# Performance work log

Measured on AMD Instinct MI355X. Metric: run time of the kernel, lower is better.

## Reference

```python
import jax, jax.numpy as jnp
import numpy as np

N_HEAD = 16
TEMPERATURE = 1.0

def setup_inputs() -> dict:
    key = jax.random.key(0)
    ks = jax.random.split(key, 5)
    B, L, D = 2, 2048, 1024
    s = 0.02
    return {
        'x':     jax.random.normal(ks[0], (B, L, D), jnp.float32),
        'q_g':   jax.random.normal(ks[1], (B, L, D), jnp.float32),
        'k_g':   jax.random.normal(ks[2], (B, L, D), jnp.float32),
        'W_qkv': jax.random.normal(ks[3], (D, 3 * D), jnp.float32) * s,
        'W_out': jax.random.normal(ks[4], (D, D), jnp.float32) * s,
    }

def reference(x, q_g, k_g, W_qkv, W_out):
    B, L, D = x.shape
    H = N_HEAD
    hd = D // H
    qkv = x @ W_qkv                                    # [B, L, 3D]
    q, k, v = jnp.split(qkv, 3, axis=-1)
    def to_heads(t):                                    # [B,L,D] -> [B,H,L,hd]
        return t.reshape(B, L, H, hd).transpose(0, 2, 1, 3)
    q, k, v = to_heads(q), to_heads(k), to_heads(v)
    qg, kg = to_heads(q_g), to_heads(k_g)

    scale = 1.0 / jnp.sqrt(jnp.float32(hd))
    # dual score matrices (same math as concat-on-head-dim then split)
    aw_x = jnp.einsum('bhqd,bhkd->bhqk', q, k) * scale    # [B,H,L,L]
    aw_g = jnp.einsum('bhqd,bhkd->bhqk', qg, kg) * scale  # [B,H,L,L]
    # sensory_attention=True, merge='add'
    attn = aw_x + aw_g

    causal = jnp.tril(jnp.ones((L, L), dtype=bool))
    attn = jnp.where(causal, attn, -jnp.inf)
    log_norm = jnp.log(jnp.float32(L))                    # softmax_log_norm=True
    attn = jax.nn.softmax(attn / (log_norm * TEMPERATURE), axis=-1)

    y = jnp.einsum('bhqk,bhkd->bhqd', attn, v)            # [B,H,L,hd]
    y = y.transpose(0, 2, 1, 3).reshape(B, L, D)
    return y @ W_out
```

## Files before the change

kernel.cpp:

```cpp
#include <hip/hip_runtime.h>

typedef __attribute__((ext_vector_type(8))) short bf16x8;
typedef __attribute__((ext_vector_type(4))) float f32x4;

static __device__ __forceinline__ unsigned short f2bf(float f) {
    unsigned int u = __float_as_uint(f);
    u += 0x7fffu + ((u >> 16) & 1u);
    return (unsigned short)(u >> 16);
}
static __device__ __forceinline__ unsigned int pack2bf(float lo, float hi) {
    return ((__float_as_uint(lo) + 0x8000u) >> 16) |
           ((__float_as_uint(hi) + 0x8000u) & 0xffff0000u);
}
static __device__ __forceinline__ float bf2f(short v) {
    return __uint_as_float(((unsigned int)(unsigned short)v) << 16);
}
static __device__ __forceinline__ bf16x8 cvt8v(const float* p) {
    f32x4 a = *(const f32x4*)p, b = *(const f32x4*)(p + 4);
    bf16x8 r;
    r[0] = (short)f2bf(a[0]); r[1] = (short)f2bf(a[1]);
    r[2] = (short)f2bf(a[2]); r[3] = (short)f2bf(a[3]);
    r[4] = (short)f2bf(b[0]); r[5] = (short)f2bf(b[1]);
    r[6] = (short)f2bf(b[2]); r[7] = (short)f2bf(b[3]);
    return r;
}
static __device__ __forceinline__ bf16x8 scale8v(bf16x8 v, float s) {
    bf16x8 r;
    #pragma unroll
    for (int j = 0; j < 8; ++j) r[j] = (short)f2bf(bf2f(v[j]) * s);
    return r;
}
static __device__ __forceinline__ uint4 cvt8(const float* p) {
    bf16x8 r = cvt8v(p);
    union { bf16x8 v; uint4 u; } c; c.v = r; return c.u;
}
static __device__ __forceinline__ void glds16(const unsigned short* g, unsigned short* l) {
    __builtin_amdgcn_global_load_lds(
        (const __attribute__((address_space(1))) unsigned int*)g,
        (__attribute__((address_space(3))) unsigned int*)l, 16, 0, 0);
}

static __device__ __forceinline__ void transpose_tile(
    const float* __restrict__ src, unsigned short* __restrict__ dst,
    int R, int C, int bx, int by, int tid)
{
    __shared__ unsigned short t[64 * 72];
    const int r0 = by * 64, c0 = bx * 64;
    #pragma unroll
    for (int i = 0; i < 4; ++i) {
        int idx = tid + i * 256;
        int row = idx >> 4, seg = idx & 15;
        f32x4 v = *(const f32x4*)&src[(size_t)(r0 + row) * C + c0 + seg * 4];
        #pragma unroll
        for (int j = 0; j < 4; ++j) t[row * 72 + seg * 4 + j] = f2bf(v[j]);
    }
    __syncthreads();
    #pragma unroll
    for (int i = 0; i < 2; ++i) {
        int idx = tid + i * 256;
        int row = idx >> 3, seg = idx & 7;
        uint4 tv; unsigned short* tmp = (unsigned short*)&tv;
        #pragma unroll
        for (int j = 0; j < 8; ++j) tmp[j] = t[(seg * 8 + j) * 72 + row];
        *(uint4*)&dst[(size_t)(c0 + row) * R + r0 + seg * 8] = tv;
    }
}

__global__ __launch_bounds__(256) void prep_all(
    const float* __restrict__ x, unsigned short* __restrict__ x_bf,
    const float* __restrict__ kg, unsigned short* __restrict__ kg_bf,
    const float* __restrict__ Wq, unsigned short* __restrict__ wtq,
    const float* __restrict__ Wo, unsigned short* __restrict__ wto)
{
    const int t = blockIdx.x, tid = threadIdx.x;
    if (t < 2048) {
        size_t j = ((size_t)t * 256 + tid) * 8;
        *(uint4*)&x_bf[j] = cvt8(&x[j]);
    } else if (t < 4096) {
        size_t j = ((size_t)(t - 2048) * 256 + tid) * 8;
        *(uint4*)&kg_bf[j] = cvt8(&kg[j]);
    } else if (t < 4864) {
        int tt = t - 4096;
        transpose_tile(Wq, wtq, 1024, 3072, tt % 48, tt / 48, tid);
    } else {
        int tt = t - 4864;
        transpose_tile(Wo, wto, 1024, 1024, tt & 15, tt >> 4, tid);
    }
}

__global__ __launch_bounds__(256) void gemm_qkv(
    const unsigned short* __restrict__ A, const unsigned short* __restrict__ Bt,
    unsigned short* __restrict__ qk, unsigned short* __restrict__ vt)
{
    const int K = 1024;
    __shared__ unsigned short As[128 * 32];
    __shared__ unsigned short Bs[128 * 32];
    __shared__ unsigned short Tb[128 * 136];
    const int tid = threadIdx.x;
    const int wave = tid >> 6, lane = tid & 63, quad = lane >> 4, l16 = lane & 15;
    const int wr = (wave >> 1) * 64, wc = (wave & 1) * 64;
    const int m0 = blockIdx.y * 128, n0 = blockIdx.x * 128;

    const unsigned short* ga = A  + (size_t)(m0 + wave * 32 + (lane >> 2)) * K + (lane & 3) * 8;
    const unsigned short* gb = Bt + (size_t)(n0 + wave * 32 + (lane >> 2)) * K + (lane & 3) * 8;
    unsigned short* la = &As[wave * 32 * 32];
    unsigned short* lb = &Bs[wave * 32 * 32];
    const size_t step16 = (size_t)16 * K;

    f32x4 acc[4][4];
    #pragma unroll
    for (int i = 0; i < 4; ++i)
        #pragma unroll
        for (int j = 0; j < 4; ++j) acc[i][j] = (f32x4){0.f, 0.f, 0.f, 0.f};

    for (int kt = 0; kt < K; kt += 32) {
        glds16(ga, la); glds16(ga + step16, la + 512);
        glds16(gb, lb); glds16(gb + step16, lb + 512);
        ga += 32; gb += 32;
        __syncthreads();
        bf16x8 af[4], bf[4];
        #pragma unroll
        for (int i = 0; i < 4; ++i) {
            af[i] = *(const bf16x8*)&As[(wr + i * 16 + l16) * 32 + quad * 8];
            bf[i] = *(const bf16x8*)&Bs[(wc + i * 16 + l16) * 32 + quad * 8];
        }
        #pragma unroll
        for (int mi = 0; mi < 4; ++mi)
            #pragma unroll
            for (int ni = 0; ni < 4; ++ni)
                acc[mi][ni] = __builtin_amdgcn_mfma_f32_16x16x32_bf16(
                    af[mi], bf[ni], acc[mi][ni], 0, 0, 0);
        __syncthreads();
    }

    if (blockIdx.x < 16) {
        #pragma unroll
        for (int mi = 0; mi < 4; ++mi)
            #pragma unroll
            for (int ni = 0; ni < 4; ++ni)
                #pragma unroll
                for (int r = 0; r < 4; ++r) {
                    int row = m0 + wr + mi * 16 + quad * 4 + r;
                    int col = n0 + wc + ni * 16 + l16;
                    qk[(size_t)row * 2048 + col] = f2bf(acc[mi][ni][r]);
                }
    } else {
        __syncthreads();
        #pragma unroll
        for (int mi = 0; mi < 4; ++mi)
            #pragma unroll
            for (int ni = 0; ni < 4; ++ni)
                #pragma unroll
                for (int r = 0; r < 4; ++r) {
                    int col = wc + ni * 16 + l16;
                    int row = wr + mi * 16 + quad * 4 + r;
                    Tb[col * 136 + row] = f2bf(acc[mi][ni][r]);
                }
        __syncthreads();
        const int col = tid >> 1, r0 = (tid & 1) * 64;
        const int bh = (m0 >> 11) * 16 + ((int)blockIdx.x - 16) * 2 + (col >> 6);
        size_t base = ((size_t)bh * 64 + (col & 63)) * 2048 + (m0 & 2047) + r0;
        #pragma unroll
        for (int k = 0; k < 8; ++k)
            *(uint4*)&vt[base + k * 8] = *(const uint4*)&Tb[col * 136 + r0 + k * 8];
    }
}

__global__ __launch_bounds__(256) void gemm_n64(
    const unsigned short* __restrict__ A, const unsigned short* __restrict__ Bt,
    float* __restrict__ C)
{
    const int K = 1024, N = 1024;
    __shared__ unsigned short As[128 * 32];
    __shared__ unsigned short Bs[64 * 32];
    const int tid = threadIdx.x;
    const int wave = tid >> 6, lane = tid & 63, quad = lane >> 4, l16 = lane & 15;
    const int wr = (wave >> 1) * 64, wc = (wave & 1) * 32;
    const int m0 = blockIdx.y * 128, n0 = blockIdx.x * 64;

    const unsigned short* ga = A  + (size_t)(m0 + wave * 32 + (lane >> 2)) * K + (lane & 3) * 8;
    const unsigned short* gb = Bt + (size_t)(n0 + wave * 16 + (lane >> 2)) * K + (lane & 3) * 8;
    unsigned short* la = &As[wave * 32 * 32];
    unsigned short* lb = &Bs[wave * 16 * 32];
    const size_t step16 = (size_t)16 * K;

    f32x4 acc[4][2];
    #pragma unroll
    for (int i = 0; i < 4; ++i)
        #pragma unroll
        for (int j = 0; j < 2; ++j) acc[i][j] = (f32x4){0.f, 0.f, 0.f, 0.f};

    for (int kt = 0; kt < K; kt += 32) {
        glds16(ga, la); glds16(ga + step16, la + 512);
        glds16(gb, lb);
        ga += 32; gb += 32;
        __syncthreads();
        bf16x8 af[4], bf[2];
        #pragma unroll
        for (int i = 0; i < 4; ++i)
            af[i] = *(const bf16x8*)&As[(wr + i * 16 + l16) * 32 + quad * 8];
        #pragma unroll
        for (int i = 0; i < 2; ++i)
            bf[i] = *(const bf16x8*)&Bs[(wc + i * 16 + l16) * 32 + quad * 8];
        #pragma unroll
        for (int mi = 0; mi < 4; ++mi)
            #pragma unroll
            for (int ni = 0; ni < 2; ++ni)
                acc[mi][ni] = __builtin_amdgcn_mfma_f32_16x16x32_bf16(
                    af[mi], bf[ni], acc[mi][ni], 0, 0, 0);
        __syncthreads();
    }
    #pragma unroll
    for (int mi = 0; mi < 4; ++mi)
        #pragma unroll
        for (int ni = 0; ni < 2; ++ni)
            #pragma unroll
            for (int r = 0; r < 4; ++r) {
                int row = m0 + wr + mi * 16 + quad * 4 + r;
                int col = n0 + wc + ni * 16 + l16;
                C[(size_t)row * N + col] = acc[mi][ni][r];
            }
}

template<bool DIAG>
static __device__ __forceinline__ void attn_tile(
    const unsigned short* __restrict__ Kc, const unsigned short* __restrict__ Gc,
    const unsigned short* __restrict__ Vc, unsigned short* __restrict__ Pw,
    const bf16x8 (&qf)[2][2], const bf16x8 (&gf)[2][2],
    f32x4 (&o)[2][4], float (&lsum)[2],
    int rb, int swz0, int swz1, int pxr, int quad, int l16, int wave, int reld)
{
    auto pstore = [&](int qj, int ni, unsigned long long v) {
        *(unsigned long long*)&Pw[(qj * 16 + l16) * 64 + (quad & 1) * 4 +
                                  (((ni * 2 + (quad >> 1)) ^ pxr) * 8)] = v;
    };

    #pragma unroll
    for (int ni = 0; ni < 4; ++ni) {
        const int kbase = (DIAG ? reld * 64 : 0) + ni * 16;
        if (DIAG && kbase > wave * 32 + 31) {
            pstore(0, ni, 0ull); pstore(1, ni, 0ull);
            continue;
        }
        bf16x8 kf0 = *(const bf16x8*)((const char*)Kc + rb + swz0 + ni * 2048);
        bf16x8 kf1 = *(const bf16x8*)((const char*)Kc + rb + swz1 + ni * 2048);
        bf16x8 gb0 = *(const bf16x8*)((const char*)Gc + rb + swz0 + ni * 2048);
        bf16x8 gb1 = *(const bf16x8*)((const char*)Gc + rb + swz1 + ni * 2048);
        #pragma unroll
        for (int qj = 0; qj < 2; ++qj) {
            const int qtop = wave * 32 + qj * 16;
            if (DIAG && kbase > qtop + 15) {
                pstore(qj, ni, 0ull);
                continue;
            }
            f32x4 a = (f32x4){0.f, 0.f, 0.f, 0.f};
            a = __builtin_amdgcn_mfma_f32_16x16x32_bf16(kf0, qf[qj][0], a, 0, 0, 0);
            a = __builtin_amdgcn_mfma_f32_16x16x32_bf16(gb0, gf[qj][0], a, 0, 0, 0);
            a = __builtin_amdgcn_mfma_f32_16x16x32_bf16(kf1, qf[qj][1], a, 0, 0, 0);
            a = __builtin_amdgcn_mfma_f32_16x16x32_bf16(gb1, gf[qj][1], a, 0, 0, 0);
            float e0, e1, e2, e3;
            if (DIAG && (kbase + 15 > qtop)) {
                const int qr = qtop + l16, kb = kbase + quad * 4;
                e0 = (kb + 0 <= qr) ? exp2f(a[0]) : 0.f;
                e1 = (kb + 1 <= qr) ? exp2f(a[1]) : 0.f;
                e2 = (kb + 2 <= qr) ? exp2f(a[2]) : 0.f;
                e3 = (kb + 3 <= qr) ? exp2f(a[3]) : 0.f;
            } else {
                e0 = exp2f(a[0]); e1 = exp2f(a[1]);
                e2 = exp2f(a[2]); e3 = exp2f(a[3]);
            }
            lsum[qj] += (e0 + e1) + (e2 + e3);
            unsigned int p01 = pack2bf(e0, e1), p23 = pack2bf(e2, e3);
            pstore(qj, ni, ((unsigned long long)p23 << 32) | p01);
        }
    }

    bf16x8 vf[4][2];
    #pragma unroll
    for (int nd = 0; nd < 4; ++nd) {
        vf[nd][0] = *(const bf16x8*)((const char*)Vc + rb + swz0 + nd * 2048);
        vf[nd][1] = *(const bf16x8*)((const char*)Vc + rb + swz1 + nd * 2048);
    }
    asm volatile("s_waitcnt lgkmcnt(0)" ::: "memory");

    bf16x8 pa[2][2];
    #pragma unroll
    for (int qj = 0; qj < 2; ++qj)
        #pragma unroll
        for (int c = 0; c < 2; ++c)
            pa[qj][c] = *(const bf16x8*)&Pw[(qj * 16 + l16) * 64 +
                                            (((c * 4 + quad) ^ pxr) * 8)];
    #pragma unroll
    for (int nd = 0; nd < 4; ++nd) {
        o[0][nd] = __builtin_amdgcn_mfma_f32_16x16x32_bf16(pa[0][0], vf[nd][0], o[0][nd], 0, 0, 0);
        o[0][nd] = __builtin_amdgcn_mfma_f32_16x16x32_bf16(pa[0][1], vf[nd][1], o[0][nd], 0, 0, 0);
        o[1][nd] = __builtin_amdgcn_mfma_f32_16x16x32_bf16(pa[1][0], vf[nd][0], o[1][nd], 0, 0, 0);
        o[1][nd] = __builtin_amdgcn_mfma_f32_16x16x32_bf16(pa[1][1], vf[nd][1], o[1][nd], 0, 0, 0);
    }
}

__global__ __launch_bounds__(256, 2) void attn8(
    const unsigned short* __restrict__ qk, const float* __restrict__ qg,
    const unsigned short* __restrict__ kgb, const unsigned short* __restrict__ vt,
    unsigned short* __restrict__ y)
{
    const int L = 2048, DS = 2048, Dm = 1024;
    const float SC2 = 0.125f * 1.44269504088896f / 7.6246189861593985f;

    const int yb = (int)blockIdx.y;
    const int qt = (yb < 8) ? (15 - yb) : (yb - 8);
    const int bh = blockIdx.x, b = bh >> 4, h = bh & 15;
    const int tid = threadIdx.x, wave = tid >> 6, lane = tid & 63;
    const int quad = lane >> 4, l16 = lane & 15;

    __shared__ unsigned short K_l[2][4096];
    __shared__ unsigned short G_l[2][4096];
    __shared__ unsigned short V_l[2][4096];
    __shared__ unsigned short P_l[8192];
    unsigned short* Pw = &P_l[wave * 2048];

    bf16x8 qf[2][2], gf[2][2];
    const int qrow0 = qt * 128 + wave * 32;
    #pragma unroll
    for (int qj = 0; qj < 2; ++qj) {
        const unsigned short* qp = qk + (size_t)(b * L + qrow0 + qj * 16 + l16) * DS + h * 64;
        const float* gp = qg + (size_t)(b * L + qrow0 + qj * 16 + l16) * Dm + h * 64;
        #pragma unroll
        for (int c = 0; c < 2; ++c) {
            qf[qj][c] = scale8v(*(const bf16x8*)(qp + c * 32 + quad * 8), SC2);
            gf[qj][c] = scale8v(cvt8v(gp + c * 32 + quad * 8), SC2);
        }
    }

    f32x4 o[2][4];
    #pragma unroll
    for (int qj = 0; qj < 2; ++qj)
        #pragma unroll
        for (int nd = 0; nd < 4; ++nd) o[qj][nd] = (f32x4){0.f, 0.f, 0.f, 0.f};
    float lsum[2] = {0.f, 0.f};

    const int srow = wave * 16 + (lane >> 3);
    const int c8 = (((lane & 7) ^ (lane >> 3)) & 7) * 8;
    const unsigned short* pk = qk + (size_t)(b * L + srow) * DS + 1024 + h * 64 + c8;
    const unsigned short* pg = kgb + (size_t)(b * L + srow) * Dm + h * 64 + c8;
    const unsigned short* pv = vt + ((size_t)bh * 64 + srow) * L + c8;

    auto STAGE = [&](int bi) {
        unsigned short* lK = &K_l[bi][wave * 1024];
        unsigned short* lG = &G_l[bi][wave * 1024];
        unsigned short* lV = &V_l[bi][wave * 1024];
        glds16(pk, lK); glds16(pk + 8 * DS, lK + 512);
        glds16(pg, lG); glds16(pg + 8 * Dm, lG + 512);
        glds16(pv, lV); glds16(pv + 8 * L,  lV + 512);
        pk += 64 * DS; pg += 64 * Dm; pv += 64;
    };

    const int rb = l16 * 128;
    const int swz0 = ((quad ^ (l16 & 7)) * 16);
    const int swz1 = (((4 + quad) ^ (l16 & 7)) * 16);
    const int pxr = l16 & 7;

    STAGE(0);
    int cur = 0;

    for (int kt = 0; kt < 2 * qt; ++kt) {
        asm volatile("s_waitcnt vmcnt(0)" ::: "memory");
        __syncthreads();
        STAGE(cur ^ 1);
        attn_tile<false>(&K_l[cur][0], &G_l[cur][0], &V_l[cur][0], Pw,
                         qf, gf, o, lsum, rb, swz0, swz1, pxr, quad, l16, wave, 0);
        cur ^= 1;
    }

    #pragma unroll
    for (int d = 0; d < 2; ++d) {
        asm volatile("s_waitcnt vmcnt(0)" ::: "memory");
        __syncthreads();
        if (d == 0) STAGE(cur ^ 1);
        if (!(d == 1 && wave < 2))
            attn_tile<true>(&K_l[cur][0], &G_l[cur][0], &V_l[cur][0], Pw,
                            qf, gf, o, lsum, rb, swz0, swz1, pxr, quad, l16, wave, d);
        cur ^= 1;
    }

    #pragma unroll
    for (int qj = 0; qj < 2; ++qj) {
        float rs = lsum[qj];
        rs += __shfl_xor(rs, 16);
        rs += __shfl_xor(rs, 32);
        #pragma unroll
        for (int r = 0; r < 4; ++r) {
            float inv = 1.f / __shfl(rs, (lane & 48) | (quad * 4 + r));
            int row = qt * 128 + wave * 32 + qj * 16 + quad * 4 + r;
            #pragma unroll
            for (int nd = 0; nd < 4; ++nd)
                y[(size_t)(b * L + row) * Dm + h * 64 + nd * 16 + l16] =
                    f2bf(o[qj][nd][r] * inv);
        }
    }
}

extern "C" void kernel_launch(void* const* d_in, const int* in_sizes, int n_in,
                              void* d_out, int out_size, void* d_ws, size_t ws_size,
                              hipStream_t stream) {
    const float* x     = (const float*)d_in[0];
    const float* q_g   = (const float*)d_in[1];
    const float* k_g   = (const float*)d_in[2];
    const float* W_qkv = (const float*)d_in[3];
    const float* W_out = (const float*)d_in[4];
    float* out = (float*)d_out;
    unsigned short* ws = (unsigned short*)d_ws;

    unsigned short* qk_ws = ws;
    unsigned short* y_ws  = ws + 8388608;
    unsigned short* wtq   = ws + 12582912;
    unsigned short* wto   = ws + 15728640;
    unsigned short* kg_bf = ws + 16777216;
    unsigned short* x_bf  = ws + 20971520;
    unsigned short* vt_bf = ws + 25165824;

    dim3 blk(256);
    prep_all<<<5120, blk, 0, stream>>>(x, x_bf, k_g, kg_bf, W_qkv, wtq, W_out, wto);
    gemm_qkv<<<dim3(24, 32), blk, 0, stream>>>(x_bf, wtq, qk_ws, vt_bf);
    attn8<<<dim3(32, 16), blk, 0, stream>>>(qk_ws, q_g, kg_bf, vt_bf, y_ws);
    gemm_n64<<<dim3(16, 32), blk, 0, stream>>>(y_ws, wto, out);
}
```

Before: 240.1 us.

## Shrink attention blocks to 64 query rows with two waves, single-buffered

The attention kernel moves from 256-thread blocks covering 128 query rows to 128-thread blocks covering 64 rows, doubling the grid to 32x32. The K/G/V double buffer becomes a single buffer with a barrier before and after each load. A single diagonal tile now replaces the two-step diagonal handling, and blocks are ordered with the longest causal rows first. The aim is finer-grained load balance and more resident blocks per CU, at the cost of losing load/compute overlap and reading each K/V tile for half as many query rows.

```diff
diff --git a/kernel.cpp b/kernel.cpp
--- a/kernel.cpp
+++ b/kernel.cpp
@@ -228,7 +228,7 @@
     const unsigned short* __restrict__ Vc, unsigned short* __restrict__ Pw,
     const bf16x8 (&qf)[2][2], const bf16x8 (&gf)[2][2],
     f32x4 (&o)[2][4], float (&lsum)[2],
-    int rb, int swz0, int swz1, int pxr, int quad, int l16, int wave, int reld)
+    int rb, int swz0, int swz1, int pxr, int quad, int l16, int wave)
 {
     auto pstore = [&](int qj, int ni, unsigned long long v) {
         *(unsigned long long*)&Pw[(qj * 16 + l16) * 64 + (quad & 1) * 4 +
@@ -237,7 +237,7 @@
 
     #pragma unroll
     for (int ni = 0; ni < 4; ++ni) {
-        const int kbase = (DIAG ? reld * 64 : 0) + ni * 16;
+        const int kbase = ni * 16;
         if (DIAG && kbase > wave * 32 + 31) {
             pstore(0, ni, 0ull); pstore(1, ni, 0ull);
             continue;
@@ -299,7 +299,7 @@
     }
 }
 
-__global__ __launch_bounds__(256, 2) void attn8(
+__global__ __launch_bounds__(128, 3) void attn9(
     const unsigned short* __restrict__ qk, const float* __restrict__ qg,
     const unsigned short* __restrict__ kgb, const unsigned short* __restrict__ vt,
     unsigned short* __restrict__ y)
@@ -307,20 +307,19 @@
     const int L = 2048, DS = 2048, Dm = 1024;
     const float SC2 = 0.125f * 1.44269504088896f / 7.6246189861593985f;
 
-    const int yb = (int)blockIdx.y;
-    const int qt = (yb < 8) ? (15 - yb) : (yb - 8);
+    const int qt = 31 - (int)blockIdx.y;
     const int bh = blockIdx.x, b = bh >> 4, h = bh & 15;
     const int tid = threadIdx.x, wave = tid >> 6, lane = tid & 63;
     const int quad = lane >> 4, l16 = lane & 15;
 
-    __shared__ unsigned short K_l[2][4096];
-    __shared__ unsigned short G_l[2][4096];
-    __shared__ unsigned short V_l[2][4096];
-    __shared__ unsigned short P_l[8192];
+    __shared__ unsigned short K_l[4096];
+    __shared__ unsigned short G_l[4096];
+    __shared__ unsigned short V_l[4096];
+    __shared__ unsigned short P_l[4096];
     unsigned short* Pw = &P_l[wave * 2048];
 
     bf16x8 qf[2][2], gf[2][2];
-    const int qrow0 = qt * 128 + wave * 32;
+    const int qrow0 = qt * 64 + wave * 32;
     #pragma unroll
     for (int qj = 0; qj < 2; ++qj) {
         const unsigned short* qp = qk + (size_t)(b * L + qrow0 + qj * 16 + l16) * DS + h * 64;
@@ -339,48 +338,45 @@
         for (int nd = 0; nd < 4; ++nd) o[qj][nd] = (f32x4){0.f, 0.f, 0.f, 0.f};
     float lsum[2] = {0.f, 0.f};
 
-    const int srow = wave * 16 + (lane >> 3);
+    const int srow = wave * 32 + (lane >> 3);
     const int c8 = (((lane & 7) ^ (lane >> 3)) & 7) * 8;
     const unsigned short* pk = qk + (size_t)(b * L + srow) * DS + 1024 + h * 64 + c8;
     const unsigned short* pg = kgb + (size_t)(b * L + srow) * Dm + h * 64 + c8;
     const unsigned short* pv = vt + ((size_t)bh * 64 + srow) * L + c8;
-
-    auto STAGE = [&](int bi) {
-        unsigned short* lK = &K_l[bi][wave * 1024];
-        unsigned short* lG = &G_l[bi][wave * 1024];
-        unsigned short* lV = &V_l[bi][wave * 1024];
-        glds16(pk, lK); glds16(pk + 8 * DS, lK + 512);
-        glds16(pg, lG); glds16(pg + 8 * Dm, lG + 512);
-        glds16(pv, lV); glds16(pv + 8 * L,  lV + 512);
-        pk += 64 * DS; pg += 64 * Dm; pv += 64;
-    };
+    unsigned short* lK = &K_l[wave * 2048];
+    unsigned short* lG = &G_l[wave * 2048];
+    unsigned short* lV = &V_l[wave * 2048];
 
     const int rb = l16 * 128;
-    const int swz0 = ((quad ^ (l16 & 7)) * 16);
+    const int swz0 = ((quad     ^ (l16 & 7)) * 16);
     const int swz1 = (((4 + quad) ^ (l16 & 7)) * 16);
     const int pxr = l16 & 7;
 
-    STAGE(0);
-    int cur = 0;
-
-    for (int kt = 0; kt < 2 * qt; ++kt) {
-        asm volatile("s_waitcnt vmcnt(0)" ::: "memory");
-        __syncthreads();
-        STAGE(cur ^ 1);
-        attn_tile<false>(&K_l[cur][0], &G_l[cur][0], &V_l[cur][0], Pw,
-                         qf, gf, o, lsum, rb, swz0, swz1, pxr, quad, l16, wave, 0);
-        cur ^= 1;
-    }
-
-    #pragma unroll
-    for (int d = 0; d < 2; ++d) {
-        asm volatile("s_waitcnt vmcnt(0)" ::: "memory");
-        __syncthreads();
-        if (d == 0) STAGE(cur ^ 1);
-        if (!(d == 1 && wave < 2))
-            attn_tile<true>(&K_l[cur][0], &G_l[cur][0], &V_l[cur][0], Pw,
-                            qf, gf, o, lsum, rb, swz0, swz1, pxr, quad, l16, wave, d);
-        cur ^= 1;
+    for (int kt = 0; kt < qt; ++kt) {
+        __syncthreads();
+        glds16(pk, lK); glds16(pk +  8 * DS, lK + 512);
+        glds16(pk + 16 * DS, lK + 1024); glds16(pk + 24 * DS, lK + 1536);
+        glds16(pg, lG); glds16(pg +  8 * Dm, lG + 512);
+        glds16(pg + 16 * Dm, lG + 1024); glds16(pg + 24 * Dm, lG + 1536);
+        glds16(pv, lV); glds16(pv +  8 * L,  lV + 512);
+        glds16(pv + 16 * L, lV + 1024); glds16(pv + 24 * L, lV + 1536);
+        pk += 64 * DS; pg += 64 * Dm; pv += 64;
+        __syncthreads();
+        attn_tile<false>(K_l, G_l, V_l, Pw, qf, gf, o, lsum,
+                         rb, swz0, swz1, pxr, quad, l16, wave);
+    }
+
+    {
+        __syncthreads();
+        glds16(pk, lK); glds16(pk +  8 * DS, lK + 512);
+        glds16(pk + 16 * DS, lK + 1024); glds16(pk + 24 * DS, lK + 1536);
+        glds16(pg, lG); glds16(pg +  8 * Dm, lG + 512);
+        glds16(pg + 16 * Dm, lG + 1024); glds16(pg + 24 * Dm, lG + 1536);
+        glds16(pv, lV); glds16(pv +  8 * L,  lV + 512);
+        glds16(pv + 16 * L, lV + 1024); glds16(pv + 24 * L, lV + 1536);
+        __syncthreads();
+        attn_tile<true>(K_l, G_l, V_l, Pw, qf, gf, o, lsum,
+                        rb, swz0, swz1, pxr, quad, l16, wave);
     }
 
     #pragma unroll
@@ -391,7 +387,7 @@
         #pragma unroll
         for (int r = 0; r < 4; ++r) {
             float inv = 1.f / __shfl(rs, (lane & 48) | (quad * 4 + r));
-            int row = qt * 128 + wave * 32 + qj * 16 + quad * 4 + r;
+            int row = qt * 64 + wave * 32 + qj * 16 + quad * 4 + r;
             #pragma unroll
             for (int nd = 0; nd < 4; ++nd)
                 y[(size_t)(b * L + row) * Dm + h * 64 + nd * 16 + l16] =
@@ -422,6 +418,6 @@
     dim3 blk(256);
     prep_all<<<5120, blk, 0, stream>>>(x, x_bf, k_g, kg_bf, W_qkv, wtq, W_out, wto);
     gemm_qkv<<<dim3(24, 32), blk, 0, stream>>>(x_bf, wtq, qk_ws, vt_bf);
-    attn8<<<dim3(32, 16), blk, 0, stream>>>(qk_ws, q_g, kg_bf, vt_bf, y_ws);
+    attn9<<<dim3(32, 32), dim3(128), 0, stream>>>(qk_ws, q_g, kg_bf, vt_bf, y_ws);
     gemm_n64<<<dim3(16, 32), blk, 0, stream>>>(y_ws, wto, out);
 }
```

Result: no change. 241.6 us (+0.6%).
